# Kernel tuning notes

Hardware: AMD Instinct MI355X
Metric: run time of the kernel (lower is better)

Reference implementation:

```python
import jax, jax.numpy as jnp
import numpy as np

B, Q, C, H, D, E, I = 8, 256, 192, 20, 64, 1500, 5120
HID = H * D  # 1280
EPS = 1e-5
SCALE = D ** -0.5


def _linear(x, w, b):
    return jnp.einsum('bsh,oh->bso', x, w) + b


def _layernorm(x, w, b):
    xf = x.astype(jnp.float32)
    mu = jnp.mean(xf, axis=-1, keepdims=True)
    var = jnp.mean(jnp.square(xf - mu), axis=-1, keepdims=True)
    return ((xf - mu) * jax.lax.rsqrt(var + EPS) * w + b).astype(x.dtype)


def _heads(x):  # [B,S,HID] -> [B,H,S,D]
    return x.reshape(B, -1, H, D).transpose(0, 2, 1, 3)


def setup_inputs() -> dict:
    key = jax.random.key(0)
    ks = jax.random.split(key, 24)
    s = 0.02
    inp = {
        'hidden_states': jax.random.normal(ks[0], (B, Q, HID), jnp.float32),
        'mask': jnp.zeros((B, 1, Q, Q + C), jnp.float32),
        'past_key': jax.random.normal(ks[1], (B, H, C, D), jnp.float32),
        'past_value': jax.random.normal(ks[2], (B, H, C, D), jnp.float32),
        'cross_key': jax.random.normal(ks[3], (B, H, E, D), jnp.float32),
        'cross_value': jax.random.normal(ks[4], (B, H, E, D), jnp.float32),
        'q_w': jax.random.normal(ks[5], (HID, HID), jnp.float32) * s,
        'q_b': jnp.zeros((HID,), jnp.float32),
        'k_w': jax.random.normal(ks[6], (HID, HID), jnp.float32) * s,
        'k_b': jnp.zeros((HID,), jnp.float32),
        'v_w': jax.random.normal(ks[7], (HID, HID), jnp.float32) * s,
        'v_b': jnp.zeros((HID,), jnp.float32),
        'o_w': jax.random.normal(ks[8], (HID, HID), jnp.float32) * s,
        'o_b': jnp.zeros((HID,), jnp.float32),
        'cq_w': jax.random.normal(ks[9], (HID, HID), jnp.float32) * s,
        'cq_b': jnp.zeros((HID,), jnp.float32),
        'co_w': jax.random.normal(ks[10], (HID, HID), jnp.float32) * s,
        'co_b': jnp.zeros((HID,), jnp.float32),
        'up_w': jax.random.normal(ks[11], (I, HID), jnp.float32) * s,
        'up_b': jnp.zeros((I,), jnp.float32),
        'down_w': jax.random.normal(ks[12], (HID, I), jnp.float32) * s,
        'down_b': jnp.zeros((HID,), jnp.float32),
        'ln1_w': jnp.ones((HID,), jnp.float32),
        'ln1_b': jnp.zeros((HID,), jnp.float32),
        'ln2_w': jnp.ones((HID,), jnp.float32),
        'ln2_b': jnp.zeros((HID,), jnp.float32),
        'ln3_w': jnp.ones((HID,), jnp.float32),
        'ln3_b': jnp.zeros((HID,), jnp.float32),
    }
    return inp


def reference(hidden_states, mask, past_key, past_value, cross_key, cross_value,
              q_w, q_b, k_w, k_b, v_w, v_b, o_w, o_b,
              cq_w, cq_b, co_w, co_b, up_w, up_b, down_w, down_b,
              ln1_w, ln1_b, ln2_w, ln2_b, ln3_w, ln3_b):
    # ---- self-attention block ----
    residual = hidden_states
    x = _layernorm(hidden_states, ln1_w, ln1_b)
    q = _heads(_linear(x, q_w, q_b) * SCALE)          # [B,H,Q,D]
    k_new = _heads(_linear(x, k_w, k_b))              # [B,H,Q,D]
    v_new = _heads(_linear(x, v_w, v_b))
    k = jnp.concatenate([past_key, k_new], axis=2)    # [B,H,C+Q,D]
    v = jnp.concatenate([past_value, v_new], axis=2)
    scores = jnp.einsum('bhqd,bhkd->bhqk', q, k) + mask
    attn = jnp.einsum('bhqk,bhkd->bhqd', jax.nn.softmax(scores, axis=-1), v)
    attn = attn.transpose(0, 2, 1, 3).reshape(B, Q, HID)
    attn_out = _linear(attn, o_w, o_b)
    present_key = k[:, :, Q:, :]
    present_value = v[:, :, Q:, :]
    h = residual + attn_out
    # ---- cross-attention block ----
    residual = h
    x = _layernorm(h, ln2_w, ln2_b)
    cq = _heads(_linear(x, cq_w, cq_b) * SCALE)       # [B,H,Q,D]
    cscores = jnp.einsum('bhqd,bhkd->bhqk', cq, cross_key)
    cattn = jnp.einsum('bhqk,bhkd->bhqd', jax.nn.softmax(cscores, axis=-1), cross_value)
    cattn = cattn.transpose(0, 2, 1, 3).reshape(B, Q, HID)
    h = residual + _linear(cattn, co_w, co_b)
    # ---- MLP block ----
    residual = h
    x = _layernorm(h, ln3_w, ln3_b)
    up = _linear(x, up_w, up_b)
    mlp_out = _linear(jax.nn.gelu(up, approximate=False), down_w, down_b)
    h = residual + mlp_out
    return (h, present_key, present_value)
```

## Files before the change

### kernel.cpp

```cpp
#include <hip/hip_runtime.h>
#include <math.h>

#define Bc   8
#define Qn   256
#define Cn   192
#define Hn   20
#define Dn   64
#define En   1500
#define In   5120
#define HIDn 1280
#define BQ   2048
#define KSELF 448
#define EPAD 1536
#define S1   (BQ*HIDn)
#define WSZ  (HIDn*HIDn)
#define BH   (Bc*Hn)

typedef __attribute__((ext_vector_type(8))) short bf16x8;
typedef __attribute__((ext_vector_type(4))) float f32x4;

__device__ __forceinline__ short f2bf(float f) {
  union { float f; unsigned u; } x; x.f = f;
  unsigned r = x.u + 0x7fffu + ((x.u >> 16) & 1u);
  return (short)(r >> 16);
}
__device__ __forceinline__ float bf2f(short s) {
  union { unsigned u; float f; } x; x.u = ((unsigned)(unsigned short)s) << 16;
  return x.f;
}
__device__ __forceinline__ void gload16(const short* g, short* l) {
  __builtin_amdgcn_global_load_lds(
      (const __attribute__((address_space(1))) void*)g,
      (__attribute__((address_space(3))) void*)l, 16, 0, 0);
}
__device__ __forceinline__ bf16x8 cvt8(const float* p) {
  const float4 a = *reinterpret_cast<const float4*>(p);
  const float4 b = *reinterpret_cast<const float4*>(p + 4);
  bf16x8 t;
  t[0] = f2bf(a.x); t[1] = f2bf(a.y); t[2] = f2bf(a.z); t[3] = f2bf(a.w);
  t[4] = f2bf(b.x); t[5] = f2bf(b.y); t[6] = f2bf(b.z); t[7] = f2bf(b.w);
  return t;
}

__global__ __launch_bounds__(256) void convert_all(
    const float* q, const float* k, const float* v, const float* o,
    const float* cq, const float* co, const float* up, const float* dn,
    short* wq, short* wk, short* wv, short* wo,
    short* wcq, short* wco, short* wup, short* wdn)
{
  const float* src; short* dst; int n;
  switch (blockIdx.y) {
    case 0: src = q;  dst = wq;  n = WSZ; break;
    case 1: src = k;  dst = wk;  n = WSZ; break;
    case 2: src = v;  dst = wv;  n = WSZ; break;
    case 3: src = o;  dst = wo;  n = WSZ; break;
    case 4: src = cq; dst = wcq; n = WSZ; break;
    case 5: src = co; dst = wco; n = WSZ; break;
    case 6: src = up; dst = wup; n = HIDn * In; break;
    default: src = dn; dst = wdn; n = HIDn * In; break;
  }
  const int i = (blockIdx.x * 256 + threadIdx.x) * 8;
  if (i >= n) return;
  *reinterpret_cast<bf16x8*>(dst + i) = cvt8(src + i);
}

__global__ __launch_bounds__(256) void prep_cross(
    const float* __restrict__ K, const float* __restrict__ V,
    short* __restrict__ Kc, short* __restrict__ Vc)
{
  const size_t idx = (size_t)blockIdx.x * 256 + threadIdx.x;
  const int d8 = (int)(idx & 7) * 8;
  const size_t t = idx >> 3;
  const int key = (int)(t % EPAD);
  const int bh  = (int)(t / EPAD);
  bf16x8 kv = (bf16x8)0, vv = (bf16x8)0;
  if (key < En) {
    const size_t off = ((size_t)bh * En + key) * 64 + d8;
    kv = cvt8(K + off);
    vv = cvt8(V + off);
  }
  const size_t dst = ((size_t)bh * EPAD + key) * 64 + d8;
  *reinterpret_cast<bf16x8*>(Kc + dst) = kv;
  *reinterpret_cast<bf16x8*>(Vc + dst) = vv;
}

__global__ __launch_bounds__(256) void prep_self(
    const float* __restrict__ Kp, const float* __restrict__ Vp,
    const short* __restrict__ kn, const short* __restrict__ vn,
    short* __restrict__ Kc, short* __restrict__ Vc)
{
  const size_t idx = (size_t)blockIdx.x * 256 + threadIdx.x;
  const int d8 = (int)(idx & 7) * 8;
  const size_t t = idx >> 3;
  const int key = (int)(t % KSELF);
  const int bh  = (int)(t / KSELF);
  bf16x8 kv, vv;
  if (key < Cn) {
    const size_t off = ((size_t)bh * Cn + key) * 64 + d8;
    kv = cvt8(Kp + off);
    vv = cvt8(Vp + off);
  } else {
    const int b = bh / Hn, h = bh % Hn;
    const size_t off = ((size_t)(b * Qn + (key - Cn))) * HIDn + h * 64 + d8;
    kv = *reinterpret_cast<const bf16x8*>(kn + off);
    vv = *reinterpret_cast<const bf16x8*>(vn + off);
  }
  const size_t dst = ((size_t)bh * KSELF + key) * 64 + d8;
  *reinterpret_cast<bf16x8*>(Kc + dst) = kv;
  *reinterpret_cast<bf16x8*>(Vc + dst) = vv;
}

template<bool BFIN>
__global__ __launch_bounds__(256) void layernorm_k(
    const void* __restrict__ in, const float* __restrict__ w,
    const float* __restrict__ b, short* __restrict__ out)
{
  const int row = blockIdx.x;
  float v[5], s = 0.f, s2 = 0.f;
#pragma unroll
  for (int i = 0; i < 5; ++i) {
    const int c = threadIdx.x + 256 * i;
    float t;
    if (BFIN) t = bf2f(((const short*)in)[(size_t)row * HIDn + c]);
    else      t = ((const float*)in)[(size_t)row * HIDn + c];
    v[i] = t; s += t; s2 += t * t;
  }
#pragma unroll
  for (int off = 1; off < 64; off <<= 1) {
    s  += __shfl_xor(s,  off, 64);
    s2 += __shfl_xor(s2, off, 64);
  }
  __shared__ float red[8];
  const int wave = threadIdx.x >> 6, lane = threadIdx.x & 63;
  if (lane == 0) { red[wave] = s; red[wave + 4] = s2; }
  __syncthreads();
  s  = red[0] + red[1] + red[2] + red[3];
  s2 = red[4] + red[5] + red[6] + red[7];
  const float mu  = s / HIDn;
  const float var = s2 / HIDn - mu * mu;
  const float rs  = rsqrtf(var + 1e-5f);
#pragma unroll
  for (int i = 0; i < 5; ++i) {
    const int c = threadIdx.x + 256 * i;
    out[(size_t)row * HIDn + c] = f2bf((v[i] - mu) * rs * w[c] + b[c]);
  }
}

template<int BM, int BN, int MODE>
__global__ __launch_bounds__(512) void gemm8(
    const short* __restrict__ A, const short* __restrict__ W,
    const float* __restrict__ bias, const void* __restrict__ resid,
    void* __restrict__ out0, void* __restrict__ out1, void* __restrict__ out2,
    const float* __restrict__ b1, const float* __restrict__ b2,
    int N, int K, int LDK, float scale)
{
  static_assert(BM == 64 && BN == 128, "vmcnt literal assumes 3 loads/wave/stage");
  constexpr int FM = BM / 32, FN = BN / 64;
  constexpr int NLA = BM / 64, NLB = BN / 64;
  constexpr int ASH = BM * 64, BSH = BN * 64;
  __shared__ __align__(16) short Alds[3][ASH];
  __shared__ __align__(16) short Blds[3][BSH];
  const int tid = threadIdx.x, lane = tid & 63, wave = tid >> 6;
  const int wm = wave >> 2, wn = wave & 3;
  const int lr = lane & 15;
  const int kc = (lane >> 4) * 8;

  const int GX = gridDim.x, T = GX * gridDim.y;
  const int orig = blockIdx.x + GX * blockIdx.y;
  const int cpx = T >> 3;
  const int lid = (orig & 7) * cpx + (orig >> 3);
  const int m0 = (lid % GX) * BM;
  const int n0 = (lid / GX) * BN;

  f32x4 acc[FM][FN];
#pragma unroll
  for (int mi = 0; mi < FM; ++mi)
#pragma unroll
    for (int ni = 0; ni < FN; ++ni)
      acc[mi][ni] = (f32x4){0.f, 0.f, 0.f, 0.f};

  auto STAGE = [&](int kt, int buf) {
    const int k0 = kt << 6;
#pragma unroll
    for (int j = 0; j < NLA; ++j) {
      const int i = wave + 8 * j;
      const int rr = i >> 1, kk = i & 1;
      gload16(A + (size_t)(m0 + rr * 16 + lr) * LDK + k0 + kk * 32 + kc,
              &Alds[buf][i * 512]);
    }
#pragma unroll
    for (int j = 0; j < NLB; ++j) {
      const int i = wave + 8 * j;
      const int rr = i >> 1, kk = i & 1;
      gload16(W + (size_t)(n0 + rr * 16 + lr) * LDK + k0 + kk * 32 + kc,
              &Blds[buf][i * 512]);
    }
  };

  const int nk = K >> 6;
  STAGE(0, 0);
  STAGE(1, 1);

  int cur = 0;
  for (int kt = 0; kt < nk; ++kt) {
    if (kt + 1 < nk) asm volatile("s_waitcnt vmcnt(3)" ::: "memory");
    else             asm volatile("s_waitcnt vmcnt(0)" ::: "memory");
    __builtin_amdgcn_s_barrier();
    __builtin_amdgcn_sched_barrier(0);
    if (kt + 2 < nk) STAGE(kt + 2, cur + 2 >= 3 ? cur - 1 : cur + 2);
    bf16x8 af[2][FM], bfv[2][FN];
#pragma unroll
    for (int kk = 0; kk < 2; ++kk) {
#pragma unroll
      for (int mi = 0; mi < FM; ++mi)
        af[kk][mi] = *reinterpret_cast<const bf16x8*>(
            &Alds[cur][((wm * FM + mi) * 2 + kk) * 512 + lane * 8]);
#pragma unroll
      for (int ni = 0; ni < FN; ++ni)
        bfv[kk][ni] = *reinterpret_cast<const bf16x8*>(
            &Blds[cur][((wn * FN + ni) * 2 + kk) * 512 + lane * 8]);
    }
#pragma unroll
    for (int kk = 0; kk < 2; ++kk)
#pragma unroll
      for (int mi = 0; mi < FM; ++mi)
#pragma unroll
        for (int ni = 0; ni < FN; ++ni)
          acc[mi][ni] = __builtin_amdgcn_mfma_f32_16x16x32_bf16(
              af[kk][mi], bfv[kk][ni], acc[mi][ni], 0, 0, 0);
    __builtin_amdgcn_sched_barrier(0);
    cur = cur + 1 >= 3 ? 0 : cur + 1;
  }

  const int cn = lane & 15;
  const int rb = (lane >> 4) * 4;
  const int rg = (MODE == 3) ? n0 / 1280 : 0;
  const float* bp = (MODE == 3) ? (rg == 0 ? bias : rg == 1 ? b1 : b2) : bias;
  const float  sc = (MODE == 3) ? (rg == 0 ? 0.125f : 1.f) : scale;
  short* op3 = (MODE == 3)
      ? (rg == 0 ? (short*)out0 : rg == 1 ? (short*)out1 : (short*)out2) : nullptr;
#pragma unroll
  for (int mi = 0; mi < FM; ++mi)
#pragma unroll
    for (int ni = 0; ni < FN; ++ni)
#pragma unroll
      for (int j = 0; j < 4; ++j) {
        const int row = m0 + wm * (BM / 2) + mi * 16 + rb + j;
        const int col = n0 + wn * (BN / 4) + ni * 16 + cn;
        const float a = acc[mi][ni][j];
        if (MODE == 0) {
          ((float*)out0)[(size_t)row * N + col] =
              a + bp[col] + ((const float*)resid)[(size_t)row * N + col];
        } else if (MODE == 6) {
          ((float*)out0)[(size_t)row * N + col] =
              a + bp[col] + bf2f(((const short*)resid)[(size_t)row * N + col]);
        } else if (MODE == 5) {
          ((short*)out0)[(size_t)row * N + col] =
              f2bf(a + bp[col] + ((const float*)resid)[(size_t)row * N + col]);
        } else if (MODE == 1) {
          ((short*)out0)[(size_t)row * N + col] = f2bf((a + bp[col]) * sc);
        } else if (MODE == 2) {
          float t = a + bp[col];
          t = 0.5f * t * (1.f + erff(t * 0.70710678118654752f));
          ((short*)out0)[(size_t)row * N + col] = f2bf(t);
        } else {
          const int cl = col - rg * 1280;
          op3[(size_t)row * 1280 + cl] = f2bf((a + bp[cl]) * sc);
        }
      }
}

template<bool HASMASK>
__global__ __launch_bounds__(512) void attn_mfma(
    const short* __restrict__ Qb, const short* __restrict__ Kc,
    const short* __restrict__ Vc, const float* __restrict__ mask,
    short* __restrict__ Ob, int PADK, int KT)
{
  const int orig = blockIdx.x;
  const int idx  = (orig & 7) * 40 + (orig >> 3);
  const int qt = idx & 1;
  const int h  = (idx >> 1) % Hn;
  const int b  = idx / (2 * Hn);
  const int bh = b * Hn + h;
  const int tid = threadIdx.x, lane = tid & 63, wave = tid >> 6;
  const int q0 = qt * 128;
  const int cn = lane & 15;
  const int hg = lane >> 4;
  const int rb = hg * 4;

  __shared__ __align__(16) short k_s[64][72];
  __shared__ __align__(16) short vt_s[64][72];
  __shared__ __align__(16) short p_s[8][16][72];

  bf16x8 aq[2];
  {
    const short* qrow = Qb + (size_t)(b * Qn + q0 + wave * 16 + cn) * HIDn + h * 64;
    aq[0] = *reinterpret_cast<const bf16x8*>(qrow + hg * 8);
    aq[1] = *reinterpret_cast<const bf16x8*>(qrow + 32 + hg * 8);
  }

  float mrun[4] = {-1e30f, -1e30f, -1e30f, -1e30f};
  float lrun[4] = {0.f, 0.f, 0.f, 0.f};
  f32x4 oacc[4];
#pragma unroll
  for (int t = 0; t < 4; ++t) oacc[t] = (f32x4){0.f, 0.f, 0.f, 0.f};

  const int nchunk = PADK >> 6;
  for (int ci = 0; ci < nchunk; ++ci) {
    const int c0 = ci * 64;
    const short* kbase = Kc + ((size_t)bh * PADK + c0) * 64;
    const short* vbase = Vc + ((size_t)bh * PADK + c0) * 64;
    {
      const int i = tid;
      const int key = i >> 3, d8 = (i & 7) * 8;
      const bf16x8 kv = *reinterpret_cast<const bf16x8*>(kbase + key * 64 + d8);
      const bf16x8 vv = *reinterpret_cast<const bf16x8*>(vbase + key * 64 + d8);
      *reinterpret_cast<bf16x8*>(&k_s[key][d8]) = kv;
      const int g = key >> 3, o = key & 7, f = i & 7;
      const int col = ((g ^ f) << 3) | o;
#pragma unroll
      for (int j = 0; j < 8; ++j) vt_s[d8 + j][col] = vv[j];
    }
    __syncthreads();

    f32x4 sacc[4];
#pragma unroll
    for (int t = 0; t < 4; ++t) sacc[t] = (f32x4){0.f, 0.f, 0.f, 0.f};
#pragma unroll
    for (int t = 0; t < 4; ++t)
#pragma unroll
      for (int kk = 0; kk < 2; ++kk) {
        const bf16x8 bk = *reinterpret_cast<const bf16x8*>(&k_s[t * 16 + cn][kk * 32 + hg * 8]);
        sacc[t] = __builtin_amdgcn_mfma_f32_16x16x32_bf16(aq[kk], bk, sacc[t], 0, 0, 0);
      }

    float sc[4][4];
#pragma unroll
    for (int t = 0; t < 4; ++t) {
      const int key = c0 + t * 16 + cn;
      const bool valid = key < KT;
#pragma unroll
      for (int j = 0; j < 4; ++j) {
        float v = sacc[t][j];
        if (HASMASK && valid)
          v += mask[((size_t)(b * Qn) + q0 + wave * 16 + rb + j) * KT + key];
        sc[t][j] = valid ? v : -1e30f;
      }
    }

#pragma unroll
    for (int j = 0; j < 4; ++j) {
      float mx = fmaxf(fmaxf(sc[0][j], sc[1][j]), fmaxf(sc[2][j], sc[3][j]));
#pragma unroll
      for (int off = 1; off < 16; off <<= 1) mx = fmaxf(mx, __shfl_xor(mx, off, 64));
      if (mx > mrun[j] + 8.f) {
        const float alpha = __expf(mrun[j] - mx);
        lrun[j] *= alpha;
#pragma unroll
        for (int t = 0; t < 4; ++t) oacc[t][j] *= alpha;
        mrun[j] = mx;
      }
      float ps = 0.f;
#pragma unroll
      for (int t = 0; t < 4; ++t) {
        const float p = __expf(sc[t][j] - mrun[j]);
        sc[t][j] = p; ps += p;
      }
#pragma unroll
      for (int off = 1; off < 16; off <<= 1) ps += __shfl_xor(ps, off, 64);
      lrun[j] += ps;
    }

#pragma unroll
    for (int t = 0; t < 4; ++t)
#pragma unroll
      for (int j = 0; j < 4; ++j)
        p_s[wave][rb + j][t * 16 + cn] = f2bf(sc[t][j]);

    const bf16x8 ap0 = *reinterpret_cast<const bf16x8*>(&p_s[wave][cn][hg * 8]);
    const bf16x8 ap1 = *reinterpret_cast<const bf16x8*>(&p_s[wave][cn][32 + hg * 8]);
#pragma unroll
    for (int t = 0; t < 4; ++t) {
      const int d  = t * 16 + cn;
      const int fd = (d >> 3) & 7;
      const bf16x8 bv0 = *reinterpret_cast<const bf16x8*>(&vt_s[d][((hg)     ^ fd) << 3]);
      const bf16x8 bv1 = *reinterpret_cast<const bf16x8*>(&vt_s[d][((4 + hg) ^ fd) << 3]);
      oacc[t] = __builtin_amdgcn_mfma_f32_16x16x32_bf16(ap0, bv0, oacc[t], 0, 0, 0);
      oacc[t] = __builtin_amdgcn_mfma_f32_16x16x32_bf16(ap1, bv1, oacc[t], 0, 0, 0);
    }
    __syncthreads();
  }

#pragma unroll
  for (int t = 0; t < 4; ++t)
#pragma unroll
    for (int j = 0; j < 4; ++j)
      Ob[(size_t)(b * Qn + q0 + wave * 16 + rb + j) * HIDn + h * 64 + t * 16 + cn] =
          f2bf(oacc[t][j] / lrun[j]);
}

__global__ __launch_bounds__(256) void copy_present(
    const short* __restrict__ kn, const short* __restrict__ vn,
    float* __restrict__ outk, float* __restrict__ outv)
{
  const int idx = blockIdx.x * 256 + threadIdx.x;
  if (idx >= Bc * Hn * Cn * 8) return;
  const int d8 = (idx & 7) * 8;
  int t = idx >> 3;
  const int c = t % Cn; t /= Cn;
  const int h = t % Hn;
  const int b = t / Hn;
  const size_t src = (size_t)(b * Qn + (Qn - Cn) + c) * HIDn + h * 64 + d8;
  const size_t dst = (((size_t)b * Hn + h) * Cn + c) * 64 + d8;
  const bf16x8 kv = *reinterpret_cast<const bf16x8*>(kn + src);
  const bf16x8 vv = *reinterpret_cast<const bf16x8*>(vn + src);
#pragma unroll
  for (int j = 0; j < 8; ++j) {
    outk[dst + j] = bf2f(kv[j]);
    outv[dst + j] = bf2f(vv[j]);
  }
}

extern "C" void kernel_launch(void* const* d_in, const int* in_sizes, int n_in,
                              void* d_out, int out_size, void* d_ws, size_t ws_size,
                              hipStream_t stream)
{
  const float* hidden  = (const float*)d_in[0];
  const float* mask    = (const float*)d_in[1];
  const float* past_k  = (const float*)d_in[2];
  const float* past_v  = (const float*)d_in[3];
  const float* cross_k = (const float*)d_in[4];
  const float* cross_v = (const float*)d_in[5];
  const float* q_w  = (const float*)d_in[6];  const float* q_b  = (const float*)d_in[7];
  const float* k_w  = (const float*)d_in[8];  const float* k_b  = (const float*)d_in[9];
  const float* v_w  = (const float*)d_in[10]; const float* v_b  = (const float*)d_in[11];
  const float* o_w  = (const float*)d_in[12]; const float* o_b  = (const float*)d_in[13];
  const float* cq_w = (const float*)d_in[14]; const float* cq_b = (const float*)d_in[15];
  const float* co_w = (const float*)d_in[16]; const float* co_b = (const float*)d_in[17];
  const float* up_w = (const float*)d_in[18]; const float* up_b = (const float*)d_in[19];
  const float* dn_w = (const float*)d_in[20]; const float* dn_b = (const float*)d_in[21];
  const float* ln1w = (const float*)d_in[22]; const float* ln1b = (const float*)d_in[23];
  const float* ln2w = (const float*)d_in[24]; const float* ln2b = (const float*)d_in[25];
  const float* ln3w = (const float*)d_in[26]; const float* ln3b = (const float*)d_in[27];

  short* wq  = (short*)d_ws;
  short* wk  = wq  + (size_t)WSZ;
  short* wv  = wk  + (size_t)WSZ;
  short* wo  = wv  + (size_t)WSZ;
  short* wcq = wo  + (size_t)WSZ;
  short* wco = wcq + (size_t)WSZ;
  short* wup = wco + (size_t)WSZ;
  short* wdn = wup + (size_t)HIDn * In;
  short* xb  = wdn + (size_t)HIDn * In;
  short* qb  = xb  + (size_t)S1;
  short* kb  = qb  + (size_t)S1;
  short* vb  = kb  + (size_t)S1;
  short* ab  = vb  + (size_t)S1;
  short* U   = ab  + (size_t)S1;
  short* ksb = U;
  short* vsb = U + (size_t)BH * KSELF * 64;
  short* upa = U;
  short* kcc = U + (size_t)BQ * In;
  short* vcc = kcc + (size_t)BH * EPAD * 64;
  short* h1b = (short*)(vcc + (size_t)BH * EPAD * 64);

  float* out_h  = (float*)d_out;
  float* out_pk = out_h + (size_t)S1;
  float* out_pv = out_pk + (size_t)(Bc * Hn * Cn * Dn);
  float* h2 = out_h;

  const dim3 blk(256);
  const dim3 blk8(512);
  const dim3 gconv(3200, 8);
  const dim3 gqkv(32, 30);
  const dim3 gn64(32, 10);
  const dim3 gup(32, 40);
  const dim3 gattn(320);

  convert_all<<<gconv, blk, 0, stream>>>(q_w, k_w, v_w, o_w, cq_w, co_w, up_w, dn_w,
                                         wq, wk, wv, wo, wcq, wco, wup, wdn);
  prep_cross<<<(BH * EPAD * 8) / 256, blk, 0, stream>>>(cross_k, cross_v, kcc, vcc);
  layernorm_k<false><<<BQ, blk, 0, stream>>>(hidden, ln1w, ln1b, xb);
  gemm8<64, 128, 3><<<gqkv, blk8, 0, stream>>>(xb, wq, q_b, nullptr,
      qb, kb, vb, k_b, v_b, 3840, HIDn, HIDn, 1.f);
  copy_present<<<(Bc * Hn * Cn * 8 + 255) / 256, blk, 0, stream>>>(kb, vb, out_pk, out_pv);
  prep_self<<<(BH * KSELF * 8) / 256, blk, 0, stream>>>(past_k, past_v, kb, vb, ksb, vsb);
  attn_mfma<true><<<gattn, blk8, 0, stream>>>(qb, ksb, vsb, mask, ab, KSELF, KSELF);
  gemm8<64, 128, 5><<<gn64, blk8, 0, stream>>>(ab, wo, o_b, hidden,
      h1b, nullptr, nullptr, nullptr, nullptr, HIDn, HIDn, HIDn, 1.f);
  layernorm_k<true><<<BQ, blk, 0, stream>>>(h1b, ln2w, ln2b, xb);
  gemm8<64, 128, 1><<<gn64, blk8, 0, stream>>>(xb, wcq, cq_b, nullptr,
      qb, nullptr, nullptr, nullptr, nullptr, HIDn, HIDn, HIDn, 0.125f);
  attn_mfma<false><<<gattn, blk8, 0, stream>>>(qb, kcc, vcc, nullptr, ab, EPAD, En);
  gemm8<64, 128, 6><<<gn64, blk8, 0, stream>>>(ab, wco, co_b, h1b,
      h2, nullptr, nullptr, nullptr, nullptr, HIDn, HIDn, HIDn, 1.f);
  layernorm_k<false><<<BQ, blk, 0, stream>>>(h2, ln3w, ln3b, xb);
  gemm8<64, 128, 2><<<gup, blk8, 0, stream>>>(xb, wup, up_b, nullptr,
      upa, nullptr, nullptr, nullptr, nullptr, In, HIDn, HIDn, 1.f);
  gemm8<64, 128, 0><<<gn64, blk8, 0, stream>>>(upa, wdn, dn_b, h2,
      out_h, nullptr, nullptr, nullptr, nullptr, HIDn, In, In, 1.f);
}
```

Measured before the change: 586.5 us.

## Use larger GEMM tiles and split-K the down projection with a reduce kernel

Switches the QKV, up and down projections from 64x128 to 128x256 block tiles, raising register and LDS reuse per block and generalising the vmcnt wait to the new loads-per-stage count. The down projection (K=5120) is split into two K halves along gridDim.z. Each half writes fp32 partials into reused scratch buffers, and a new reduce kernel adds the partials, bias and residual. The aim is higher arithmetic intensity, with split-K restoring enough blocks for the down GEMM. The cost is an extra kernel with extra fp32 traffic and fewer blocks for the QKV and up GEMMs. LDS use for triple-buffered 128x256 tiles (~144KB) may also limit occupancy despite the launch-bounds hint.

```diff
diff --git a/kernel.cpp b/kernel.cpp
--- a/kernel.cpp
+++ b/kernel.cpp
@@ -147,16 +147,16 @@
 }
 
 template<int BM, int BN, int MODE>
-__global__ __launch_bounds__(512) void gemm8(
+__global__ __launch_bounds__(512, 2) void gemm8(
     const short* __restrict__ A, const short* __restrict__ W,
     const float* __restrict__ bias, const void* __restrict__ resid,
     void* __restrict__ out0, void* __restrict__ out1, void* __restrict__ out2,
     const float* __restrict__ b1, const float* __restrict__ b2,
     int N, int K, int LDK, float scale)
 {
-  static_assert(BM == 64 && BN == 128, "vmcnt literal assumes 3 loads/wave/stage");
   constexpr int FM = BM / 32, FN = BN / 64;
   constexpr int NLA = BM / 64, NLB = BN / 64;
+  constexpr int NL  = NLA + NLB;
   constexpr int ASH = BM * 64, BSH = BN * 64;
   __shared__ __align__(16) short Alds[3][ASH];
   __shared__ __align__(16) short Blds[3][BSH];
@@ -171,6 +171,8 @@
   const int lid = (orig & 7) * cpx + (orig >> 3);
   const int m0 = (lid % GX) * BM;
   const int n0 = (lid / GX) * BN;
+  const int bz = blockIdx.z;
+  const size_t koff = (size_t)bz * K;
 
   f32x4 acc[FM][FN];
 #pragma unroll
@@ -185,14 +187,14 @@
     for (int j = 0; j < NLA; ++j) {
       const int i = wave + 8 * j;
       const int rr = i >> 1, kk = i & 1;
-      gload16(A + (size_t)(m0 + rr * 16 + lr) * LDK + k0 + kk * 32 + kc,
+      gload16(A + (size_t)(m0 + rr * 16 + lr) * LDK + koff + k0 + kk * 32 + kc,
               &Alds[buf][i * 512]);
     }
 #pragma unroll
     for (int j = 0; j < NLB; ++j) {
       const int i = wave + 8 * j;
       const int rr = i >> 1, kk = i & 1;
-      gload16(W + (size_t)(n0 + rr * 16 + lr) * LDK + k0 + kk * 32 + kc,
+      gload16(W + (size_t)(n0 + rr * 16 + lr) * LDK + koff + k0 + kk * 32 + kc,
               &Blds[buf][i * 512]);
     }
   };
@@ -203,8 +205,12 @@
 
   int cur = 0;
   for (int kt = 0; kt < nk; ++kt) {
-    if (kt + 1 < nk) asm volatile("s_waitcnt vmcnt(3)" ::: "memory");
-    else             asm volatile("s_waitcnt vmcnt(0)" ::: "memory");
+    if (kt + 1 < nk) {
+      if constexpr (NL == 3) asm volatile("s_waitcnt vmcnt(3)" ::: "memory");
+      else                   asm volatile("s_waitcnt vmcnt(6)" ::: "memory");
+    } else {
+      asm volatile("s_waitcnt vmcnt(0)" ::: "memory");
+    }
     __builtin_amdgcn_s_barrier();
     __builtin_amdgcn_sched_barrier(0);
     if (kt + 2 < nk) STAGE(kt + 2, cur + 2 >= 3 ? cur - 1 : cur + 2);
@@ -263,11 +269,34 @@
           float t = a + bp[col];
           t = 0.5f * t * (1.f + erff(t * 0.70710678118654752f));
           ((short*)out0)[(size_t)row * N + col] = f2bf(t);
+        } else if (MODE == 4) {
+          float* op = bz == 0 ? (float*)out0 : (float*)out1;
+          op[(size_t)row * N + col] = a;
         } else {
           const int cl = col - rg * 1280;
           op3[(size_t)row * 1280 + cl] = f2bf((a + bp[cl]) * sc);
         }
       }
+}
+
+__global__ __launch_bounds__(256) void reduce_k(
+    const float* __restrict__ p0, const float* __restrict__ p1,
+    const float* __restrict__ resid, const float* __restrict__ bias,
+    float* __restrict__ out)
+{
+  const size_t i = ((size_t)blockIdx.x * 256 + threadIdx.x) * 4;
+  if (i >= (size_t)S1) return;
+  const int col = (int)(i % HIDn);
+  const float4 a  = *reinterpret_cast<const float4*>(p0 + i);
+  const float4 b  = *reinterpret_cast<const float4*>(p1 + i);
+  const float4 bi = *reinterpret_cast<const float4*>(bias + col);
+  const float4 r  = *reinterpret_cast<const float4*>(resid + i);
+  float4 o;
+  o.x = a.x + b.x + bi.x + r.x;
+  o.y = a.y + b.y + bi.y + r.y;
+  o.z = a.z + b.z + bi.z + r.z;
+  o.w = a.w + b.w + bi.w + r.w;
+  *reinterpret_cast<float4*>(out + i) = o;
 }
 
 template<bool HASMASK>
@@ -463,6 +492,8 @@
   short* kcc = U + (size_t)BQ * In;
   short* vcc = kcc + (size_t)BH * EPAD * 64;
   short* h1b = (short*)(vcc + (size_t)BH * EPAD * 64);
+  float* pd0 = (float*)qb;
+  float* pd1 = (float*)vb;
 
   float* out_h  = (float*)d_out;
   float* out_pk = out_h + (size_t)S1;
@@ -472,16 +503,18 @@
   const dim3 blk(256);
   const dim3 blk8(512);
   const dim3 gconv(3200, 8);
-  const dim3 gqkv(32, 30);
+  const dim3 gqkv(16, 15);
   const dim3 gn64(32, 10);
-  const dim3 gup(32, 40);
+  const dim3 gup(16, 20);
+  const dim3 gdn(16, 5, 2);
   const dim3 gattn(320);
+  const dim3 gred((S1 / 4 + 255) / 256);
 
   convert_all<<<gconv, blk, 0, stream>>>(q_w, k_w, v_w, o_w, cq_w, co_w, up_w, dn_w,
                                          wq, wk, wv, wo, wcq, wco, wup, wdn);
   prep_cross<<<(BH * EPAD * 8) / 256, blk, 0, stream>>>(cross_k, cross_v, kcc, vcc);
   layernorm_k<false><<<BQ, blk, 0, stream>>>(hidden, ln1w, ln1b, xb);
-  gemm8<64, 128, 3><<<gqkv, blk8, 0, stream>>>(xb, wq, q_b, nullptr,
+  gemm8<128, 256, 3><<<gqkv, blk8, 0, stream>>>(xb, wq, q_b, nullptr,
       qb, kb, vb, k_b, v_b, 3840, HIDn, HIDn, 1.f);
   copy_present<<<(Bc * Hn * Cn * 8 + 255) / 256, blk, 0, stream>>>(kb, vb, out_pk, out_pv);
   prep_self<<<(BH * KSELF * 8) / 256, blk, 0, stream>>>(past_k, past_v, kb, vb, ksb, vsb);
@@ -495,8 +528,9 @@
   gemm8<64, 128, 6><<<gn64, blk8, 0, stream>>>(ab, wco, co_b, h1b,
       h2, nullptr, nullptr, nullptr, nullptr, HIDn, HIDn, HIDn, 1.f);
   layernorm_k<false><<<BQ, blk, 0, stream>>>(h2, ln3w, ln3b, xb);
-  gemm8<64, 128, 2><<<gup, blk8, 0, stream>>>(xb, wup, up_b, nullptr,
+  gemm8<128, 256, 2><<<gup, blk8, 0, stream>>>(xb, wup, up_b, nullptr,
       upa, nullptr, nullptr, nullptr, nullptr, In, HIDn, HIDn, 1.f);
-  gemm8<64, 128, 0><<<gn64, blk8, 0, stream>>>(upa, wdn, dn_b, h2,
-      out_h, nullptr, nullptr, nullptr, nullptr, HIDn, In, In, 1.f);
-}
+  gemm8<128, 256, 4><<<gdn, blk8, 0, stream>>>(upa, wdn, nullptr, nullptr,
+      pd0, pd1, nullptr, nullptr, nullptr, HIDn, In / 2, In, 1.f);
+  reduce_k<<<gred, blk, 0, stream>>>(pd0, pd1, h2, dn_b, out_h);
+}
```

Result: faster. 569.9 us (-2.8%).
